# Performance work log

Hardware: AMD Instinct MI355X
Metric: run time of the kernel (lower is better)

## Reference

```python
import jax, jax.numpy as jnp
import numpy as np

H = 128            # hidden_size; also the chunk length from torch.split(x, hidden_size)
NUM_CHUNKS = 4096  # B
INPUT_SIZE = 1
NUM_CLASSES = 1


def setup_inputs() -> dict:
    key = jax.random.key(0)
    ks = jax.random.split(key, 7)
    N = NUM_CHUNKS * H
    s = 1.0 / np.sqrt(H).astype(np.float32)
    x = jax.random.normal(ks[0], (N,), dtype=jnp.float32)
    W_ih = jax.random.uniform(ks[1], (4 * H, INPUT_SIZE), minval=-s, maxval=s, dtype=jnp.float32)
    W_hh = jax.random.uniform(ks[2], (4 * H, H), minval=-s, maxval=s, dtype=jnp.float32)
    b_ih = jax.random.uniform(ks[3], (4 * H,), minval=-s, maxval=s, dtype=jnp.float32)
    b_hh = jax.random.uniform(ks[4], (4 * H,), minval=-s, maxval=s, dtype=jnp.float32)
    fc_W = jax.random.uniform(ks[5], (NUM_CLASSES, H), minval=-s, maxval=s, dtype=jnp.float32)
    fc_b = jax.random.uniform(ks[6], (NUM_CLASSES,), minval=-s, maxval=s, dtype=jnp.float32)
    return {"x": x, "W_ih": W_ih, "W_hh": W_hh, "b_ih": b_ih, "b_hh": b_hh,
            "fc_W": fc_W, "fc_b": fc_b}


def reference(x, W_ih, W_hh, b_ih, b_hh, fc_W, fc_b):
    # Original: split flat x into chunks of length H, run each chunk as a
    # batch-1 LSTM (input_size=1), take final hidden state, apply fc_out.
    # Here all chunks are batched into one fused recurrent pass.
    Hh = W_hh.shape[1]
    xb = x.reshape(-1, Hh, 1)                                  # [B, T=H, 1]
    # input projection is time-parallel: precompute gate pre-activations
    pre = jnp.einsum('bti,gi->btg', xb, W_ih) + b_ih + b_hh    # [B, T, 4H]

    def step(carry, p_t):
        h, c = carry                                           # [B, H] each
        gates = p_t + h @ W_hh.T                               # [B, 4H]
        i, f, g, o = jnp.split(gates, 4, axis=-1)              # PyTorch gate order i,f,g,o
        i = jax.nn.sigmoid(i)
        f = jax.nn.sigmoid(f)
        g = jnp.tanh(g)
        o = jax.nn.sigmoid(o)
        c = f * c + i * g
        h = o * jnp.tanh(c)
        return (h, c), None

    B = xb.shape[0]
    h0 = jnp.zeros((B, Hh), dtype=x.dtype)
    c0 = jnp.zeros((B, Hh), dtype=x.dtype)
    (hT, _), _ = jax.lax.scan(step, (h0, c0), jnp.swapaxes(pre, 0, 1))
    return hT @ fc_W.T + fc_b                                  # [B, num_classes]
```

## Files before the change

### kernel.cpp

```cpp
#include <hip/hip_runtime.h>


#define H   128
#define T   128
#define MB  16
#define BLOCK 512
#define HSTRIDE 136

typedef _Float16 f16x8 __attribute__((ext_vector_type(8)));
typedef float    f32x4 __attribute__((ext_vector_type(4)));

__device__ __forceinline__ float fsig(float v) {
    float e = __expf(-v);
    return __builtin_amdgcn_rcpf(1.0f + e);
}
__device__ __forceinline__ float ftanh(float v) {
    float e = __expf(2.0f * v);
    return 1.0f - 2.0f * __builtin_amdgcn_rcpf(1.0f + e);
}

__launch_bounds__(BLOCK, 2)
__global__ void lstm_fused_kernel(const float* __restrict__ x,
                                  const float* __restrict__ W_ih,
                                  const float* __restrict__ W_hh,
                                  const float* __restrict__ b_ih,
                                  const float* __restrict__ b_hh,
                                  const float* __restrict__ fc_W,
                                  const float* __restrict__ fc_b,
                                  float* __restrict__ out)
{
    __shared__ float xs[MB][T];
    __shared__ __align__(16) _Float16 hbuf[2][MB][HSTRIDE];

    const int tid  = threadIdx.x;
    const int wave = tid >> 6;
    const int lane = tid & 63;
    const int l15  = lane & 15;
    const int q    = lane >> 4;
    const int jcol = wave * 16 + l15;

    {
        const float4* src = (const float4*)(x + (size_t)blockIdx.x * (MB * T));
        float4* dst = (float4*)(&xs[0][0]);
        dst[tid] = src[tid];
    }
    for (int i = tid; i < MB * HSTRIDE; i += BLOCK)
        (&hbuf[0][0][0])[i] = (_Float16)0.0f;

    f16x8 wf[4][4];
    float wih[4], bias[4];
    #pragma unroll
    for (int g = 0; g < 4; ++g) {
        const int n = g * H + jcol;
        wih[g]  = W_ih[n];
        bias[g] = b_ih[n] + b_hh[n];
        #pragma unroll
        for (int kc = 0; kc < 4; ++kc) {
            const float* wp = W_hh + (size_t)n * H + kc * 32 + q * 8;
            float4 w0 = ((const float4*)wp)[0];
            float4 w1 = ((const float4*)wp)[1];
            f16x8 f;
            f[0] = (_Float16)w0.x; f[1] = (_Float16)w0.y;
            f[2] = (_Float16)w0.z; f[3] = (_Float16)w0.w;
            f[4] = (_Float16)w1.x; f[5] = (_Float16)w1.y;
            f[6] = (_Float16)w1.z; f[7] = (_Float16)w1.w;
            wf[g][kc] = f;
        }
    }

    float c[4] = {0.f, 0.f, 0.f, 0.f};

    __syncthreads();

    for (int t = 0; t < T; ++t) {
        const int rb = t & 1;
        const int wb = rb ^ 1;

        f16x8 af[4];
        #pragma unroll
        for (int kc = 0; kc < 4; ++kc)
            af[kc] = *(const f16x8*)&hbuf[rb][l15][kc * 32 + q * 8];

        f32x4 acc[4];
        #pragma unroll
        for (int g = 0; g < 4; ++g) {
            #pragma unroll
            for (int r = 0; r < 4; ++r) {
                const int b = q * 4 + r;
                acc[g][r] = xs[b][t] * wih[g] + bias[g];
            }
        }

        #pragma unroll
        for (int kc = 0; kc < 4; ++kc) {
            #pragma unroll
            for (int g = 0; g < 4; ++g)
                acc[g] = __builtin_amdgcn_mfma_f32_16x16x32_f16(af[kc], wf[g][kc], acc[g], 0, 0, 0);
        }

        #pragma unroll
        for (int r = 0; r < 4; ++r) {
            const int b = q * 4 + r;
            float ig = fsig(acc[0][r]);
            float fg = fsig(acc[1][r]);
            float gg = ftanh(acc[2][r]);
            float og = fsig(acc[3][r]);
            float cn = fg * c[r] + ig * gg;
            c[r] = cn;
            float hv = og * ftanh(cn);
            hbuf[wb][b][jcol] = (_Float16)hv;
        }
        __syncthreads();
    }

    if (tid < 256) {
        const int b    = tid >> 4;
        const int part = tid & 15;
        const _Float16* hrow = &hbuf[0][b][0];
        float s = 0.0f;
        #pragma unroll
        for (int i = 0; i < 8; ++i) {
            const int j = part * 8 + i;
            s += fc_W[j] * (float)hrow[j];
        }
        s += __shfl_xor(s, 8, 16);
        s += __shfl_xor(s, 4, 16);
        s += __shfl_xor(s, 2, 16);
        s += __shfl_xor(s, 1, 16);
        if (part == 0)
            out[blockIdx.x * MB + b] = s + fc_b[0];
    }
}

extern "C" void kernel_launch(void* const* d_in, const int* in_sizes, int n_in,
                              void* d_out, int out_size, void* d_ws, size_t ws_size,
                              hipStream_t stream)
{
    const float* x    = (const float*)d_in[0];
    const float* W_ih = (const float*)d_in[1];
    const float* W_hh = (const float*)d_in[2];
    const float* b_ih = (const float*)d_in[3];
    const float* b_hh = (const float*)d_in[4];
    const float* fc_W = (const float*)d_in[5];
    const float* fc_b = (const float*)d_in[6];
    float* out = (float*)d_out;

    const int B = in_sizes[0] / H;
    dim3 grid(B / MB);
    dim3 block(BLOCK);
    hipLaunchKernelGGL(lstm_fused_kernel, grid, block, 0, stream,
                       x, W_ih, W_hh, b_ih, b_hh, fc_W, fc_b, out);
}
```

Measured before the change: 177.9 us.

## Double block size to split LSTM gate nonlinearities across duplicated MFMA waves

Doubles the block to 16 waves. Two wave groups each compute the full recurrent MFMA for the same 16 hidden columns, but each applies the gate sigmoid/tanh and cell update to only two of the four batch rows. This shortens the per-step serial transcendental tail on the critical path, at the cost of doing all matrix-core work twice and adding more waves per SIMD. It also transposes the x staging buffer in shared memory with padding, so each step reads consecutive batch entries instead of strided rows.

```diff
diff --git a/kernel.cpp b/kernel.cpp
--- a/kernel.cpp
+++ b/kernel.cpp
@@ -4,8 +4,9 @@
 #define H   128
 #define T   128
 #define MB  16
-#define BLOCK 512
+#define BLOCK 1024
 #define HSTRIDE 136
+#define XSTRIDE 17
 
 typedef _Float16 f16x8 __attribute__((ext_vector_type(8)));
 typedef float    f32x4 __attribute__((ext_vector_type(4)));
@@ -19,7 +20,7 @@
     return 1.0f - 2.0f * __builtin_amdgcn_rcpf(1.0f + e);
 }
 
-__launch_bounds__(BLOCK, 2)
+__launch_bounds__(BLOCK, 4)
 __global__ void lstm_fused_kernel(const float* __restrict__ x,
                                   const float* __restrict__ W_ih,
                                   const float* __restrict__ W_hh,
@@ -29,20 +30,24 @@
                                   const float* __restrict__ fc_b,
                                   float* __restrict__ out)
 {
-    __shared__ float xs[MB][T];
+    __shared__ float xs[T][XSTRIDE];
     __shared__ __align__(16) _Float16 hbuf[2][MB][HSTRIDE];
 
-    const int tid  = threadIdx.x;
-    const int wave = tid >> 6;
-    const int lane = tid & 63;
-    const int l15  = lane & 15;
-    const int q    = lane >> 4;
-    const int jcol = wave * 16 + l15;
+    const int tid   = threadIdx.x;
+    const int wave  = tid >> 6;
+    const int lane  = tid & 63;
+    const int l15   = lane & 15;
+    const int q     = lane >> 4;
+    const int colw  = wave & 7;
+    const int rbase = (wave >> 3) * 2;
+    const int jcol  = colw * 16 + l15;
 
     {
-        const float4* src = (const float4*)(x + (size_t)blockIdx.x * (MB * T));
-        float4* dst = (float4*)(&xs[0][0]);
-        dst[tid] = src[tid];
+        const int t0 = tid & 127;
+        const int b0 = tid >> 7;
+        const float* xb = x + (size_t)blockIdx.x * (MB * T);
+        xs[t0][b0]     = xb[b0 * T + t0];
+        xs[t0][b0 + 8] = xb[(b0 + 8) * T + t0];
     }
     for (int i = tid; i < MB * HSTRIDE; i += BLOCK)
         (&hbuf[0][0][0])[i] = (_Float16)0.0f;
@@ -68,7 +73,7 @@
         }
     }
 
-    float c[4] = {0.f, 0.f, 0.f, 0.f};
+    float c0 = 0.f, c1 = 0.f;
 
     __syncthreads();
 
@@ -85,30 +90,38 @@
         #pragma unroll
         for (int g = 0; g < 4; ++g) {
             #pragma unroll
-            for (int r = 0; r < 4; ++r) {
-                const int b = q * 4 + r;
-                acc[g][r] = xs[b][t] * wih[g] + bias[g];
-            }
+            for (int r = 0; r < 4; ++r)
+                acc[g][r] = xs[t][q * 4 + r] * wih[g] + bias[g];
         }
 
         #pragma unroll
-        for (int kc = 0; kc < 4; ++kc) {
+        for (int g = 0; g < 4; ++g) {
             #pragma unroll
-            for (int g = 0; g < 4; ++g)
+            for (int kc = 0; kc < 4; ++kc)
                 acc[g] = __builtin_amdgcn_mfma_f32_16x16x32_f16(af[kc], wf[g][kc], acc[g], 0, 0, 0);
         }
 
-        #pragma unroll
-        for (int r = 0; r < 4; ++r) {
-            const int b = q * 4 + r;
+        {
+            const int r  = rbase;
+            const int b  = q * 4 + r;
             float ig = fsig(acc[0][r]);
             float fg = fsig(acc[1][r]);
             float gg = ftanh(acc[2][r]);
             float og = fsig(acc[3][r]);
-            float cn = fg * c[r] + ig * gg;
-            c[r] = cn;
-            float hv = og * ftanh(cn);
-            hbuf[wb][b][jcol] = (_Float16)hv;
+            float cn = fg * c0 + ig * gg;
+            c0 = cn;
+            hbuf[wb][b][jcol] = (_Float16)(og * ftanh(cn));
+        }
+        {
+            const int r  = rbase + 1;
+            const int b  = q * 4 + r;
+            float ig = fsig(acc[0][r]);
+            float fg = fsig(acc[1][r]);
+            float gg = ftanh(acc[2][r]);
+            float og = fsig(acc[3][r]);
+            float cn = fg * c1 + ig * gg;
+            c1 = cn;
+            hbuf[wb][b][jcol] = (_Float16)(og * ftanh(cn));
         }
         __syncthreads();
     }
```

Measured after the change: 248.2 us. 39.5% more time.
